# Performance work log

Measured on AMD Instinct MI355X. Metric: run time of the kernel, lower is better.

Reference implementation:

```python
import jax, jax.numpy as jnp
import numpy as np

EPS = 1e-6

def elu_fm(x):
    # elu(x) + 1
    return jax.nn.elu(x) + 1.0

def setup_inputs() -> dict:
    key = jax.random.key(0)
    k1, k2, k3 = jax.random.split(key, 3)
    N, L, H, D = 4, 4096, 16, 64
    queries = jax.random.normal(k1, (N, L, H, D), dtype=jnp.float32)
    keys = jax.random.normal(k2, (N, L, H, D), dtype=jnp.float32)
    values = jax.random.normal(k3, (N, L, H, D), dtype=jnp.float32)
    key_mask = jnp.ones((N, L), dtype=jnp.float32)
    return {"queries": queries, "keys": keys, "values": values, "key_mask": key_mask}

def reference(queries, keys, values, key_mask):
    Q = elu_fm(queries)                                  # [n, l, h, d]
    K = elu_fm(keys) * key_mask[:, :, None, None]        # [n, s, h, d]
    # KV accumulation: outer products of keys and values summed over sequence
    KV = jnp.einsum('nshd,nshm->nhmd', K, values)        # [n, h, m, d]
    # Normalizer: Q . sum_s K
    Z = 1.0 / (jnp.einsum('nlhd,nhd->nlh', Q, K.sum(axis=1)) + EPS)
    V = jnp.einsum('nlhd,nhmd,nlh->nlhm', Q, KV, Z)      # [n, l, h, m]
    return V
```

## Files before the change

kernel.cpp:

```cpp
#include <hip/hip_runtime.h>

#define EPS 1e-6f

typedef __attribute__((ext_vector_type(8))) short short8;
typedef __attribute__((ext_vector_type(16))) float f32x16;

__device__ __forceinline__ float elu1(float x) {
    return x > 0.f ? x + 1.f : __expf(x);
}

__device__ __forceinline__ short f2bf(float x) {
    unsigned u = __float_as_uint(x);
    return (short)((u + 0x7FFFu + ((u >> 16) & 1u)) >> 16);
}

#define LGKMCNT0() asm volatile("s_waitcnt lgkmcnt(0)" ::: "memory")
#define BAR() do { LGKMCNT0(); __builtin_amdgcn_s_barrier(); \
                   asm volatile("" ::: "memory"); } while (0)

template<int ITERS>
__global__ __launch_bounds__(256, 2) void kv_partial_kernel(
    const float* __restrict__ keys, const float* __restrict__ values,
    const float* __restrict__ mask, float* __restrict__ pkv,
    float* __restrict__ pks)
{
    __shared__ float Kls[64][64];
    __shared__ float Vls[64][64];
    __shared__ float Mls[ITERS * 64];

    const int nh = blockIdx.x, n = nh >> 4, h = nh & 15;
    const int chunk = blockIdx.y;
    const int t = threadIdx.x, wv = t >> 6, l = t & 63;
    const int half = l >> 5, col = l & 31;
    const int r0 = t >> 4, c4 = (t & 15) * 4;

    const int s0 = chunk * (ITERS * 64);
    const float* kb = keys   + ((size_t)(n * 4096 + s0) * 16 + h) * 64;
    const float* vb = values + ((size_t)(n * 4096 + s0) * 16 + h) * 64;

    if (t < ITERS * 16)
        *(float4*)&Mls[t * 4] = *(const float4*)(mask + n * 4096 + s0 + t * 4);

    f32x16 acc[2][2];
    #pragma unroll
    for (int a = 0; a < 2; ++a)
        #pragma unroll
        for (int b = 0; b < 2; ++b)
            #pragma unroll
            for (int r = 0; r < 16; ++r) acc[a][b][r] = 0.f;
    float4 ks4 = make_float4(0.f, 0.f, 0.f, 0.f);

    float4 kr[4], vr[4];
    #pragma unroll
    for (int k = 0; k < 4; ++k) {
        const size_t go = (size_t)(r0 + 16 * k) * 1024 + c4;
        kr[k] = *(const float4*)(kb + go);
        vr[k] = *(const float4*)(vb + go);
    }

    #pragma unroll
    for (int it = 0; it < ITERS; ++it) {
        BAR();
        #pragma unroll
        for (int k = 0; k < 4; ++k) {
            const float msk = Mls[it * 64 + r0 + 16 * k];
            float4 kk = kr[k];
            kk.x = elu1(kk.x) * msk; kk.y = elu1(kk.y) * msk;
            kk.z = elu1(kk.z) * msk; kk.w = elu1(kk.w) * msk;
            ks4.x += kk.x; ks4.y += kk.y; ks4.z += kk.z; ks4.w += kk.w;
            *(float4*)&Kls[r0 + 16 * k][c4] = kk;
            *(float4*)&Vls[r0 + 16 * k][c4] = vr[k];
        }
        BAR();
        if (it + 1 < ITERS) {
            #pragma unroll
            for (int k = 0; k < 4; ++k) {
                const size_t go = (size_t)(r0 + 16 * k + 64 * (it + 1)) * 1024 + c4;
                kr[k] = *(const float4*)(kb + go);
                vr[k] = *(const float4*)(vb + go);
            }
        }
        short8 ka0, ka1, va0, va1;
        #pragma unroll
        for (int j = 0; j < 8; ++j) {
            const int s = 16 * wv + 8 * half + j;
            ka0[j] = f2bf(Kls[s][col]);
            ka1[j] = f2bf(Kls[s][col + 32]);
            va0[j] = f2bf(Vls[s][col]);
            va1[j] = f2bf(Vls[s][col + 32]);
        }
        acc[0][0] = __builtin_amdgcn_mfma_f32_32x32x16_bf16(ka0, va0, acc[0][0], 0, 0, 0);
        acc[0][1] = __builtin_amdgcn_mfma_f32_32x32x16_bf16(ka0, va1, acc[0][1], 0, 0, 0);
        acc[1][0] = __builtin_amdgcn_mfma_f32_32x32x16_bf16(ka1, va0, acc[1][0], 0, 0, 0);
        acc[1][1] = __builtin_amdgcn_mfma_f32_32x32x16_bf16(ka1, va1, acc[1][1], 0, 0, 0);
    }

    BAR();
    *(float4*)&Kls[r0][c4] = ks4;
    BAR();
    if (t < 64) {
        float s = 0.f;
        #pragma unroll
        for (int r = 0; r < 16; ++r) s += Kls[r][t];
        pks[((size_t)chunk * 64 + nh) * 64 + t] = s;
    }
    BAR();

    float* cb0 = &Kls[0][0];
    float* cb1 = &Vls[0][0];
#define FLATW(BUF)                                                         \
    { _Pragma("unroll") for (int td = 0; td < 2; ++td)                     \
      _Pragma("unroll") for (int tm = 0; tm < 2; ++tm)                     \
      _Pragma("unroll") for (int r = 0; r < 16; ++r)                       \
          BUF[((td * 2 + tm) * 16 + r) * 64 + l] = acc[td][tm][r]; }
#define FLATR(BUF)                                                         \
    { _Pragma("unroll") for (int td = 0; td < 2; ++td)                     \
      _Pragma("unroll") for (int tm = 0; tm < 2; ++tm)                     \
      _Pragma("unroll") for (int r = 0; r < 16; ++r)                       \
          acc[td][tm][r] += BUF[((td * 2 + tm) * 16 + r) * 64 + l]; }
    if (wv == 2) FLATW(cb0);
    if (wv == 3) FLATW(cb1);
    BAR();
    if (wv == 0) FLATR(cb0);
    if (wv == 1) FLATR(cb1);
    BAR();
    if (wv == 1) FLATW(cb0);
    BAR();
    if (wv == 0) {
        FLATR(cb0);
        float* pb = pkv + ((size_t)chunk * 64 + nh) * 4096;
        #pragma unroll
        for (int td = 0; td < 2; ++td)
            #pragma unroll
            for (int tm = 0; tm < 2; ++tm)
                #pragma unroll
                for (int r = 0; r < 16; ++r) {
                    const int d = 32 * td + (r & 3) + 8 * (r >> 2) + 4 * half;
                    pb[(size_t)d * 64 + 32 * tm + col] = acc[td][tm][r];
                }
    }
#undef FLATW
#undef FLATR
}

__global__ __launch_bounds__(256) void kv_reduce_kernel(
    const float* __restrict__ pkv, const float* __restrict__ pks,
    float* __restrict__ kvt, float* __restrict__ ksum, int CH)
{
    const int nh = blockIdx.x;
    const int f4 = blockIdx.y * 256 + threadIdx.x;
    float4 s4 = make_float4(0.f, 0.f, 0.f, 0.f);
    #pragma unroll 4
    for (int c = 0; c < CH; ++c) {
        const float4 v = *(const float4*)(pkv + ((size_t)c * 64 + nh) * 4096 + f4 * 4);
        s4.x += v.x; s4.y += v.y; s4.z += v.z; s4.w += v.w;
    }
    *(float4*)(kvt + (size_t)nh * 4096 + f4 * 4) = s4;

    if (blockIdx.y == 0 && threadIdx.x < 64) {
        float s = 0.f;
        #pragma unroll 4
        for (int c = 0; c < CH; ++c)
            s += pks[((size_t)c * 64 + nh) * 64 + threadIdx.x];
        ksum[nh * 64 + threadIdx.x] = s;
    }
}

__global__ __launch_bounds__(256) void out_kernel(
    const float* __restrict__ queries, const float* __restrict__ kvt,
    const float* __restrict__ ksum, float* __restrict__ out)
{
    __shared__ float Qs[64][68];
    __shared__ float KVs[64][68];
    __shared__ float Ksm[64];

    const int nh = blockIdx.x;
    const int n = nh >> 4, h = nh & 15;
    const int t = threadIdx.x;
    const int l0 = blockIdx.y * 64;

    #pragma unroll
    for (int k = 0; k < 4; ++k) {
        const int idx = t + k * 256;
        *(float4*)&KVs[idx >> 4][(idx & 15) * 4] =
            *(const float4*)(kvt + (size_t)nh * 4096 + idx * 4);
    }
    if (t < 64) Ksm[t] = ksum[nh * 64 + t];

    #pragma unroll
    for (int k = 0; k < 4; ++k) {
        const int idx = t + k * 256;
        const int row = idx >> 4, seg = idx & 15;
        const size_t g = ((size_t)(n * 4096 + l0 + row) * 16 + h) * 64 + seg * 4;
        float4 q4 = *(const float4*)(queries + g);
        q4.x = elu1(q4.x);
        q4.y = elu1(q4.y);
        q4.z = elu1(q4.z);
        q4.w = elu1(q4.w);
        *(float4*)&Qs[row][seg * 4] = q4;
    }
    __syncthreads();

    const int mg = t & 7;
    const int lg = t >> 3;

    float acc[2][8];
    float zacc[2] = {0.f, 0.f};
    #pragma unroll
    for (int i = 0; i < 2; ++i)
        #pragma unroll
        for (int j = 0; j < 8; ++j) acc[i][j] = 0.f;

    #pragma unroll 4
    for (int d0 = 0; d0 < 64; d0 += 4) {
        const float4 km4 = *(const float4*)&Ksm[d0];
        float4 q[2];
        q[0] = *(const float4*)&Qs[lg][d0];
        q[1] = *(const float4*)&Qs[lg + 32][d0];
        #pragma unroll
        for (int i = 0; i < 2; ++i)
            zacc[i] += q[i].x * km4.x + q[i].y * km4.y +
                       q[i].z * km4.z + q[i].w * km4.w;
        #pragma unroll
        for (int r = 0; r < 4; ++r) {
            const float4 kva = *(const float4*)&KVs[d0 + r][mg * 4];
            const float4 kvb = *(const float4*)&KVs[d0 + r][32 + mg * 4];
            #pragma unroll
            for (int i = 0; i < 2; ++i) {
                const float qc = ((const float*)&q[i])[r];
                acc[i][0] = fmaf(qc, kva.x, acc[i][0]);
                acc[i][1] = fmaf(qc, kva.y, acc[i][1]);
                acc[i][2] = fmaf(qc, kva.z, acc[i][2]);
                acc[i][3] = fmaf(qc, kva.w, acc[i][3]);
                acc[i][4] = fmaf(qc, kvb.x, acc[i][4]);
                acc[i][5] = fmaf(qc, kvb.y, acc[i][5]);
                acc[i][6] = fmaf(qc, kvb.z, acc[i][6]);
                acc[i][7] = fmaf(qc, kvb.w, acc[i][7]);
            }
        }
    }

    #pragma unroll
    for (int i = 0; i < 2; ++i) {
        const float z = 1.f / (zacc[i] + EPS);
        const int row = l0 + lg + 32 * i;
        const size_t g = ((size_t)(n * 4096 + row) * 16 + h) * 64;
        float4 o;
        o.x = acc[i][0] * z; o.y = acc[i][1] * z;
        o.z = acc[i][2] * z; o.w = acc[i][3] * z;
        *(float4*)(out + g + mg * 4) = o;
        o.x = acc[i][4] * z; o.y = acc[i][5] * z;
        o.z = acc[i][6] * z; o.w = acc[i][7] * z;
        *(float4*)(out + g + 32 + mg * 4) = o;
    }
}

extern "C" void kernel_launch(void* const* d_in, const int* in_sizes, int n_in,
                              void* d_out, int out_size, void* d_ws, size_t ws_size,
                              hipStream_t stream) {
    const float* queries = (const float*)d_in[0];
    const float* keys    = (const float*)d_in[1];
    const float* values  = (const float*)d_in[2];
    const float* mask    = (const float*)d_in[3];
    float* out = (float*)d_out;

    auto need = [](int CH) {
        return ((size_t)CH * 64 * 4096 + (size_t)CH * 64 * 64 +
                (size_t)64 * 4096 + 64 * 64) * sizeof(float);
    };
    const int CH = (need(16) <= ws_size) ? 16 : 8;

    float* pkv  = (float*)d_ws;
    float* pks  = pkv + (size_t)CH * 64 * 4096;
    float* kvt  = pks + (size_t)CH * 64 * 64;
    float* ksum = kvt + (size_t)64 * 4096;

    if (CH == 16)
        kv_partial_kernel<4><<<dim3(64, 16), 256, 0, stream>>>(keys, values, mask, pkv, pks);
    else
        kv_partial_kernel<8><<<dim3(64, 8), 256, 0, stream>>>(keys, values, mask, pkv, pks);
    kv_reduce_kernel<<<dim3(64, 4), 256, 0, stream>>>(pkv, pks, kvt, ksum, CH);
    out_kernel<<<dim3(64, 64), 256, 0, stream>>>(queries, kvt, ksum, out);
}
```

Measured before the change: 79.76 us.

## Split KV accumulation into more sequence chunks and drop register prefetch pipeline

Raises the number of sequence chunks in the KV partial kernel from 16 to 64, so each block handles one 64-row tile, giving 4096 blocks instead of 1024. The register double-buffered prefetch and the shared-memory mask staging are removed; each iteration now loads its keys, values and mask straight from global memory, and the custom barrier macro is replaced with __syncthreads. The aim is more parallelism to hide memory latency on the bandwidth-bound partial pass. In exchange, the partial-KV workspace written to memory and read back by the reduce kernel grows fourfold, and each block pays a larger fixed epilogue cost for its cross-wave reduction.

New measurement: 103.6 us. +29.9%, slower.

```diff
diff --git a/kernel.cpp b/kernel.cpp
--- a/kernel.cpp
+++ b/kernel.cpp
@@ -13,10 +13,6 @@
     unsigned u = __float_as_uint(x);
     return (short)((u + 0x7FFFu + ((u >> 16) & 1u)) >> 16);
 }
-
-#define LGKMCNT0() asm volatile("s_waitcnt lgkmcnt(0)" ::: "memory")
-#define BAR() do { LGKMCNT0(); __builtin_amdgcn_s_barrier(); \
-                   asm volatile("" ::: "memory"); } while (0)
 
 template<int ITERS>
 __global__ __launch_bounds__(256, 2) void kv_partial_kernel(
@@ -26,7 +22,6 @@
 {
     __shared__ float Kls[64][64];
     __shared__ float Vls[64][64];
-    __shared__ float Mls[ITERS * 64];
 
     const int nh = blockIdx.x, n = nh >> 4, h = nh & 15;
     const int chunk = blockIdx.y;
@@ -37,9 +32,7 @@
     const int s0 = chunk * (ITERS * 64);
     const float* kb = keys   + ((size_t)(n * 4096 + s0) * 16 + h) * 64;
     const float* vb = values + ((size_t)(n * 4096 + s0) * 16 + h) * 64;
-
-    if (t < ITERS * 16)
-        *(float4*)&Mls[t * 4] = *(const float4*)(mask + n * 4096 + s0 + t * 4);
+    const float* mb = mask + n * 4096 + s0;
 
     f32x16 acc[2][2];
     #pragma unroll
@@ -50,36 +43,31 @@
             for (int r = 0; r < 16; ++r) acc[a][b][r] = 0.f;
     float4 ks4 = make_float4(0.f, 0.f, 0.f, 0.f);
 
-    float4 kr[4], vr[4];
-    #pragma unroll
-    for (int k = 0; k < 4; ++k) {
-        const size_t go = (size_t)(r0 + 16 * k) * 1024 + c4;
-        kr[k] = *(const float4*)(kb + go);
-        vr[k] = *(const float4*)(vb + go);
-    }
-
     #pragma unroll
     for (int it = 0; it < ITERS; ++it) {
-        BAR();
+        float4 kr[4], vr[4];
+        float mr[4];
         #pragma unroll
         for (int k = 0; k < 4; ++k) {
-            const float msk = Mls[it * 64 + r0 + 16 * k];
+            const int row = r0 + 16 * k;
+            const size_t go = (size_t)(it * 64 + row) * 1024 + c4;
+            kr[k] = *(const float4*)(kb + go);
+            vr[k] = *(const float4*)(vb + go);
+            mr[k] = mb[it * 64 + row];
+        }
+        if (it) __syncthreads();
+        #pragma unroll
+        for (int k = 0; k < 4; ++k) {
+            const int row = r0 + 16 * k;
             float4 kk = kr[k];
+            const float msk = mr[k];
             kk.x = elu1(kk.x) * msk; kk.y = elu1(kk.y) * msk;
             kk.z = elu1(kk.z) * msk; kk.w = elu1(kk.w) * msk;
             ks4.x += kk.x; ks4.y += kk.y; ks4.z += kk.z; ks4.w += kk.w;
-            *(float4*)&Kls[r0 + 16 * k][c4] = kk;
-            *(float4*)&Vls[r0 + 16 * k][c4] = vr[k];
-        }
-        BAR();
-        if (it + 1 < ITERS) {
-            #pragma unroll
-            for (int k = 0; k < 4; ++k) {
-                const size_t go = (size_t)(r0 + 16 * k + 64 * (it + 1)) * 1024 + c4;
-                kr[k] = *(const float4*)(kb + go);
-                vr[k] = *(const float4*)(vb + go);
-            }
-        }
+            *(float4*)&Kls[row][c4] = kk;
+            *(float4*)&Vls[row][c4] = vr[k];
+        }
+        __syncthreads();
         short8 ka0, ka1, va0, va1;
         #pragma unroll
         for (int j = 0; j < 8; ++j) {
@@ -95,16 +83,16 @@
         acc[1][1] = __builtin_amdgcn_mfma_f32_32x32x16_bf16(ka1, va1, acc[1][1], 0, 0, 0);
     }
 
-    BAR();
+    __syncthreads();
     *(float4*)&Kls[r0][c4] = ks4;
-    BAR();
+    __syncthreads();
     if (t < 64) {
         float s = 0.f;
         #pragma unroll
         for (int r = 0; r < 16; ++r) s += Kls[r][t];
         pks[((size_t)chunk * 64 + nh) * 64 + t] = s;
     }
-    BAR();
+    __syncthreads();
 
     float* cb0 = &Kls[0][0];
     float* cb1 = &Vls[0][0];
@@ -120,12 +108,12 @@
           acc[td][tm][r] += BUF[((td * 2 + tm) * 16 + r) * 64 + l]; }
     if (wv == 2) FLATW(cb0);
     if (wv == 3) FLATW(cb1);
-    BAR();
+    __syncthreads();
     if (wv == 0) FLATR(cb0);
     if (wv == 1) FLATR(cb1);
-    BAR();
+    __syncthreads();
     if (wv == 1) FLATW(cb0);
-    BAR();
+    __syncthreads();
     if (wv == 0) {
         FLATR(cb0);
         float* pb = pkv + ((size_t)chunk * 64 + nh) * 4096;
@@ -268,17 +256,17 @@
         return ((size_t)CH * 64 * 4096 + (size_t)CH * 64 * 64 +
                 (size_t)64 * 4096 + 64 * 64) * sizeof(float);
     };
-    const int CH = (need(16) <= ws_size) ? 16 : 8;
+    const int CH = (need(64) <= ws_size) ? 64 : 32;
 
     float* pkv  = (float*)d_ws;
     float* pks  = pkv + (size_t)CH * 64 * 4096;
     float* kvt  = pks + (size_t)CH * 64 * 64;
     float* ksum = kvt + (size_t)64 * 4096;
 
-    if (CH == 16)
-        kv_partial_kernel<4><<<dim3(64, 16), 256, 0, stream>>>(keys, values, mask, pkv, pks);
+    if (CH == 64)
+        kv_partial_kernel<1><<<dim3(64, 64), 256, 0, stream>>>(keys, values, mask, pkv, pks);
     else
-        kv_partial_kernel<8><<<dim3(64, 8), 256, 0, stream>>>(keys, values, mask, pkv, pks);
+        kv_partial_kernel<2><<<dim3(64, 32), 256, 0, stream>>>(keys, values, mask, pkv, pks);
     kv_reduce_kernel<<<dim3(64, 4), 256, 0, stream>>>(pkv, pks, kvt, ksum, CH);
     out_kernel<<<dim3(64, 64), 256, 0, stream>>>(queries, kvt, ksum, out);
 }
```

## Stage K/V as transposed bf16 in LDS and fix chunk count at 8

Applied to the files above, without the earlier changes.

K and V are now converted to bf16 once when written to shared memory, stored transposed with padding so each lane fetches its MFMA operand with two 8-byte LDS reads instead of 32 scalar float reads plus per-element conversion. Separate float buffers hold the cross-wave accumulator combine. The launcher now always uses 8 chunks of 8 iterations instead of 16 chunks when workspace allows, which halves partial-sum traffic but also halves grid parallelism in the first kernel. LDS footprint grows, which may affect occupancy at two blocks per CU.

New measurement: 73.76 us. 7.5% less time.

```diff
diff --git a/kernel.cpp b/kernel.cpp
--- a/kernel.cpp
+++ b/kernel.cpp
@@ -4,14 +4,19 @@
 
 typedef __attribute__((ext_vector_type(8))) short short8;
 typedef __attribute__((ext_vector_type(16))) float f32x16;
+typedef __attribute__((ext_vector_type(2))) unsigned int uint2v;
 
 __device__ __forceinline__ float elu1(float x) {
     return x > 0.f ? x + 1.f : __expf(x);
 }
 
-__device__ __forceinline__ short f2bf(float x) {
+__device__ __forceinline__ unsigned f2bfu(float x) {
     unsigned u = __float_as_uint(x);
-    return (short)((u + 0x7FFFu + ((u >> 16) & 1u)) >> 16);
+    return (u + 0x7FFFu + ((u >> 16) & 1u)) >> 16;
+}
+
+__device__ __forceinline__ float fidx(const float4& v, int i) {
+    return i == 0 ? v.x : i == 1 ? v.y : i == 2 ? v.z : v.w;
 }
 
 #define LGKMCNT0() asm volatile("s_waitcnt lgkmcnt(0)" ::: "memory")
@@ -24,8 +29,9 @@
     const float* __restrict__ mask, float* __restrict__ pkv,
     float* __restrict__ pks)
 {
-    __shared__ float Kls[64][64];
-    __shared__ float Vls[64][64];
+    __shared__ __align__(16) unsigned short KVbt[2][64][68];
+    __shared__ float cmbA[4096];
+    __shared__ float cmbB[4096];
     __shared__ float Mls[ITERS * 64];
 
     const int nh = blockIdx.x, n = nh >> 4, h = nh & 15;
@@ -41,6 +47,9 @@
     if (t < ITERS * 16)
         *(float4*)&Mls[t * 4] = *(const float4*)(mask + n * 4096 + s0 + t * 4);
 
+    char* kvbase = (char*)&KVbt[0][0][0];
+    const char* lbase = kvbase + col * 136 + 32 * wv + 16 * half;
+
     f32x16 acc[2][2];
     #pragma unroll
     for (int a = 0; a < 2; ++a)
@@ -61,6 +70,7 @@
     #pragma unroll
     for (int it = 0; it < ITERS; ++it) {
         BAR();
+        float4 kt[4];
         #pragma unroll
         for (int k = 0; k < 4; ++k) {
             const float msk = Mls[it * 64 + r0 + 16 * k];
@@ -68,8 +78,18 @@
             kk.x = elu1(kk.x) * msk; kk.y = elu1(kk.y) * msk;
             kk.z = elu1(kk.z) * msk; kk.w = elu1(kk.w) * msk;
             ks4.x += kk.x; ks4.y += kk.y; ks4.z += kk.z; ks4.w += kk.w;
-            *(float4*)&Kls[r0 + 16 * k][c4] = kk;
-            *(float4*)&Vls[r0 + 16 * k][c4] = vr[k];
+            kt[k] = kk;
+        }
+        #pragma unroll
+        for (int i = 0; i < 4; ++i) {
+            uint2v kw, vw;
+            kw[0] = f2bfu(fidx(kt[0], i)) | (f2bfu(fidx(kt[1], i)) << 16);
+            kw[1] = f2bfu(fidx(kt[2], i)) | (f2bfu(fidx(kt[3], i)) << 16);
+            vw[0] = f2bfu(fidx(vr[0], i)) | (f2bfu(fidx(vr[1], i)) << 16);
+            vw[1] = f2bfu(fidx(vr[2], i)) | (f2bfu(fidx(vr[3], i)) << 16);
+            const int bo = (c4 + i) * 136 + 8 * r0;
+            *(uint2v*)(kvbase + bo) = kw;
+            *(uint2v*)(kvbase + 8704 + bo) = vw;
         }
         BAR();
         if (it + 1 < ITERS) {
@@ -80,34 +100,35 @@
                 vr[k] = *(const float4*)(vb + go);
             }
         }
-        short8 ka0, ka1, va0, va1;
-        #pragma unroll
-        for (int j = 0; j < 8; ++j) {
-            const int s = 16 * wv + 8 * half + j;
-            ka0[j] = f2bf(Kls[s][col]);
-            ka1[j] = f2bf(Kls[s][col + 32]);
-            va0[j] = f2bf(Vls[s][col]);
-            va1[j] = f2bf(Vls[s][col + 32]);
-        }
-        acc[0][0] = __builtin_amdgcn_mfma_f32_32x32x16_bf16(ka0, va0, acc[0][0], 0, 0, 0);
-        acc[0][1] = __builtin_amdgcn_mfma_f32_32x32x16_bf16(ka0, va1, acc[0][1], 0, 0, 0);
-        acc[1][0] = __builtin_amdgcn_mfma_f32_32x32x16_bf16(ka1, va0, acc[1][0], 0, 0, 0);
-        acc[1][1] = __builtin_amdgcn_mfma_f32_32x32x16_bf16(ka1, va1, acc[1][1], 0, 0, 0);
-    }
-
-    BAR();
-    *(float4*)&Kls[r0][c4] = ks4;
+        union UF { uint2v u[2]; short8 s; };
+        UF ua, ub, uc, ud;
+        ua.u[0] = *(const uint2v*)(lbase + 0);
+        ua.u[1] = *(const uint2v*)(lbase + 8);
+        ub.u[0] = *(const uint2v*)(lbase + 4352);
+        ub.u[1] = *(const uint2v*)(lbase + 4360);
+        uc.u[0] = *(const uint2v*)(lbase + 8704);
+        uc.u[1] = *(const uint2v*)(lbase + 8712);
+        ud.u[0] = *(const uint2v*)(lbase + 13056);
+        ud.u[1] = *(const uint2v*)(lbase + 13064);
+        acc[0][0] = __builtin_amdgcn_mfma_f32_32x32x16_bf16(ua.s, uc.s, acc[0][0], 0, 0, 0);
+        acc[0][1] = __builtin_amdgcn_mfma_f32_32x32x16_bf16(ua.s, ud.s, acc[0][1], 0, 0, 0);
+        acc[1][0] = __builtin_amdgcn_mfma_f32_32x32x16_bf16(ub.s, uc.s, acc[1][0], 0, 0, 0);
+        acc[1][1] = __builtin_amdgcn_mfma_f32_32x32x16_bf16(ub.s, ud.s, acc[1][1], 0, 0, 0);
+    }
+
+    BAR();
+    *(float4*)&cmbA[r0 * 64 + c4] = ks4;
     BAR();
     if (t < 64) {
         float s = 0.f;
         #pragma unroll
-        for (int r = 0; r < 16; ++r) s += Kls[r][t];
+        for (int r = 0; r < 16; ++r) s += cmbA[r * 64 + t];
         pks[((size_t)chunk * 64 + nh) * 64 + t] = s;
     }
     BAR();
 
-    float* cb0 = &Kls[0][0];
-    float* cb1 = &Vls[0][0];
+    float* cb0 = cmbA;
+    float* cb1 = cmbB;
 #define FLATW(BUF)                                                         \
     { _Pragma("unroll") for (int td = 0; td < 2; ++td)                     \
       _Pragma("unroll") for (int tm = 0; tm < 2; ++tm)                     \
@@ -227,7 +248,7 @@
             const float4 kvb = *(const float4*)&KVs[d0 + r][32 + mg * 4];
             #pragma unroll
             for (int i = 0; i < 2; ++i) {
-                const float qc = ((const float*)&q[i])[r];
+                const float qc = fidx(q[i], r);
                 acc[i][0] = fmaf(qc, kva.x, acc[i][0]);
                 acc[i][1] = fmaf(qc, kva.y, acc[i][1]);
                 acc[i][2] = fmaf(qc, kva.z, acc[i][2]);
@@ -264,21 +285,15 @@
     const float* mask    = (const float*)d_in[3];
     float* out = (float*)d_out;
 
-    auto need = [](int CH) {
-        return ((size_t)CH * 64 * 4096 + (size_t)CH * 64 * 64 +
-                (size_t)64 * 4096 + 64 * 64) * sizeof(float);
-    };
-    const int CH = (need(16) <= ws_size) ? 16 : 8;
+    const int CH = 8;
 
     float* pkv  = (float*)d_ws;
     float* pks  = pkv + (size_t)CH * 64 * 4096;
     float* kvt  = pks + (size_t)CH * 64 * 64;
     float* ksum = kvt + (size_t)64 * 4096;
 
-    if (CH == 16)
-        kv_partial_kernel<4><<<dim3(64, 16), 256, 0, stream>>>(keys, values, mask, pkv, pks);
-    else
-        kv_partial_kernel<8><<<dim3(64, 8), 256, 0, stream>>>(keys, values, mask, pkv, pks);
+    kv_partial_kernel<8><<<dim3(64, CH), 256, 0, stream>>>(keys, values, mask,
+                                                           pkv, pks);
     kv_reduce_kernel<<<dim3(64, 4), 256, 0, stream>>>(pkv, pks, kvt, ksum, CH);
     out_kernel<<<dim3(64, 64), 256, 0, stream>>>(queries, kvt, ksum, out);
 }
```

## Replace bf16 MFMA KV accumulation with fp32 register-tiled FMA outer products

Applied to the files above, without the earlier changes.

The KV partial kernel drops the bf16 MFMA path and computes the K^T V outer-product sum in fp32 with per-thread 4x4 register tiles read from padded LDS. This removes the bf16 conversion and the cross-wave LDS reduction at the end, since each thread now writes its own tile directly. The reduce kernel scatters the results back into [d][m] order. It also drops the workspace-size fallback and always uses 16 chunks. The trade is more VALU FMA work in place of matrix-core throughput, plus uncoalesced scattered stores in the reduce kernel.

After: 100.0 us. 25.4% more time.

```diff
diff --git a/kernel.cpp b/kernel.cpp
--- a/kernel.cpp
+++ b/kernel.cpp
@@ -1,17 +1,13 @@
 #include <hip/hip_runtime.h>
 
 #define EPS 1e-6f
-
-typedef __attribute__((ext_vector_type(8))) short short8;
-typedef __attribute__((ext_vector_type(16))) float f32x16;
 
 __device__ __forceinline__ float elu1(float x) {
     return x > 0.f ? x + 1.f : __expf(x);
 }
 
-__device__ __forceinline__ short f2bf(float x) {
-    unsigned u = __float_as_uint(x);
-    return (short)((u + 0x7FFFu + ((u >> 16) & 1u)) >> 16);
+__device__ __forceinline__ float fidx(const float4& v, int i) {
+    return i == 0 ? v.x : i == 1 ? v.y : i == 2 ? v.z : v.w;
 }
 
 #define LGKMCNT0() asm volatile("s_waitcnt lgkmcnt(0)" ::: "memory")
@@ -24,15 +20,15 @@
     const float* __restrict__ mask, float* __restrict__ pkv,
     float* __restrict__ pks)
 {
-    __shared__ float Kls[64][64];
-    __shared__ float Vls[64][64];
+    __shared__ float Kls[64][68];
+    __shared__ float Vls[64][68];
     __shared__ float Mls[ITERS * 64];
 
     const int nh = blockIdx.x, n = nh >> 4, h = nh & 15;
     const int chunk = blockIdx.y;
-    const int t = threadIdx.x, wv = t >> 6, l = t & 63;
-    const int half = l >> 5, col = l & 31;
+    const int t = threadIdx.x;
     const int r0 = t >> 4, c4 = (t & 15) * 4;
+    const int m0 = (t >> 4) * 4, d0 = (t & 15) * 4;
 
     const int s0 = chunk * (ITERS * 64);
     const float* kb = keys   + ((size_t)(n * 4096 + s0) * 16 + h) * 64;
@@ -41,13 +37,11 @@
     if (t < ITERS * 16)
         *(float4*)&Mls[t * 4] = *(const float4*)(mask + n * 4096 + s0 + t * 4);
 
-    f32x16 acc[2][2];
-    #pragma unroll
-    for (int a = 0; a < 2; ++a)
-        #pragma unroll
-        for (int b = 0; b < 2; ++b)
-            #pragma unroll
-            for (int r = 0; r < 16; ++r) acc[a][b][r] = 0.f;
+    float acc[4][4];
+    #pragma unroll
+    for (int i = 0; i < 4; ++i)
+        #pragma unroll
+        for (int j = 0; j < 4; ++j) acc[i][j] = 0.f;
     float4 ks4 = make_float4(0.f, 0.f, 0.f, 0.f);
 
     float4 kr[4], vr[4];
@@ -80,19 +74,19 @@
                 vr[k] = *(const float4*)(vb + go);
             }
         }
-        short8 ka0, ka1, va0, va1;
-        #pragma unroll
-        for (int j = 0; j < 8; ++j) {
-            const int s = 16 * wv + 8 * half + j;
-            ka0[j] = f2bf(Kls[s][col]);
-            ka1[j] = f2bf(Kls[s][col + 32]);
-            va0[j] = f2bf(Vls[s][col]);
-            va1[j] = f2bf(Vls[s][col + 32]);
-        }
-        acc[0][0] = __builtin_amdgcn_mfma_f32_32x32x16_bf16(ka0, va0, acc[0][0], 0, 0, 0);
-        acc[0][1] = __builtin_amdgcn_mfma_f32_32x32x16_bf16(ka0, va1, acc[0][1], 0, 0, 0);
-        acc[1][0] = __builtin_amdgcn_mfma_f32_32x32x16_bf16(ka1, va0, acc[1][0], 0, 0, 0);
-        acc[1][1] = __builtin_amdgcn_mfma_f32_32x32x16_bf16(ka1, va1, acc[1][1], 0, 0, 0);
+        #pragma unroll 4
+        for (int s = 0; s < 64; ++s) {
+            const float4 vv = *(const float4*)&Vls[s][m0];
+            const float4 kk = *(const float4*)&Kls[s][d0];
+            #pragma unroll
+            for (int i = 0; i < 4; ++i) {
+                const float vi = fidx(vv, i);
+                acc[i][0] = fmaf(vi, kk.x, acc[i][0]);
+                acc[i][1] = fmaf(vi, kk.y, acc[i][1]);
+                acc[i][2] = fmaf(vi, kk.z, acc[i][2]);
+                acc[i][3] = fmaf(vi, kk.w, acc[i][3]);
+            }
+        }
     }
 
     BAR();
@@ -104,43 +98,13 @@
         for (int r = 0; r < 16; ++r) s += Kls[r][t];
         pks[((size_t)chunk * 64 + nh) * 64 + t] = s;
     }
-    BAR();
-
-    float* cb0 = &Kls[0][0];
-    float* cb1 = &Vls[0][0];
-#define FLATW(BUF)                                                         \
-    { _Pragma("unroll") for (int td = 0; td < 2; ++td)                     \
-      _Pragma("unroll") for (int tm = 0; tm < 2; ++tm)                     \
-      _Pragma("unroll") for (int r = 0; r < 16; ++r)                       \
-          BUF[((td * 2 + tm) * 16 + r) * 64 + l] = acc[td][tm][r]; }
-#define FLATR(BUF)                                                         \
-    { _Pragma("unroll") for (int td = 0; td < 2; ++td)                     \
-      _Pragma("unroll") for (int tm = 0; tm < 2; ++tm)                     \
-      _Pragma("unroll") for (int r = 0; r < 16; ++r)                       \
-          acc[td][tm][r] += BUF[((td * 2 + tm) * 16 + r) * 64 + l]; }
-    if (wv == 2) FLATW(cb0);
-    if (wv == 3) FLATW(cb1);
-    BAR();
-    if (wv == 0) FLATR(cb0);
-    if (wv == 1) FLATR(cb1);
-    BAR();
-    if (wv == 1) FLATW(cb0);
-    BAR();
-    if (wv == 0) {
-        FLATR(cb0);
-        float* pb = pkv + ((size_t)chunk * 64 + nh) * 4096;
-        #pragma unroll
-        for (int td = 0; td < 2; ++td)
-            #pragma unroll
-            for (int tm = 0; tm < 2; ++tm)
-                #pragma unroll
-                for (int r = 0; r < 16; ++r) {
-                    const int d = 32 * td + (r & 3) + 8 * (r >> 2) + 4 * half;
-                    pb[(size_t)d * 64 + 32 * tm + col] = acc[td][tm][r];
-                }
-    }
-#undef FLATW
-#undef FLATR
+
+    float* pb = pkv + ((size_t)chunk * 64 + nh) * 4096;
+    #pragma unroll
+    for (int i = 0; i < 4; ++i)
+        #pragma unroll
+        for (int j = 0; j < 4; ++j)
+            pb[(i * 4 + j) * 256 + t] = acc[i][j];
 }
 
 __global__ __launch_bounds__(256) void kv_reduce_kernel(
@@ -155,7 +119,16 @@
         const float4 v = *(const float4*)(pkv + ((size_t)c * 64 + nh) * 4096 + f4 * 4);
         s4.x += v.x; s4.y += v.y; s4.z += v.z; s4.w += v.w;
     }
-    *(float4*)(kvt + (size_t)nh * 4096 + f4 * 4) = s4;
+    const float vals[4] = {s4.x, s4.y, s4.z, s4.w};
+    const int k = f4 >> 6;
+    const int tb = (f4 & 63) * 4;
+    #pragma unroll
+    for (int u = 0; u < 4; ++u) {
+        const int t = tb + u;
+        const int m = ((t >> 4) << 2) + (k >> 2);
+        const int d = ((t & 15) << 2) + (k & 3);
+        kvt[(size_t)nh * 4096 + d * 64 + m] = vals[u];
+    }
 
     if (blockIdx.y == 0 && threadIdx.x < 64) {
         float s = 0.f;
@@ -227,7 +200,7 @@
             const float4 kvb = *(const float4*)&KVs[d0 + r][32 + mg * 4];
             #pragma unroll
             for (int i = 0; i < 2; ++i) {
-                const float qc = ((const float*)&q[i])[r];
+                const float qc = fidx(q[i], r);
                 acc[i][0] = fmaf(qc, kva.x, acc[i][0]);
                 acc[i][1] = fmaf(qc, kva.y, acc[i][1]);
                 acc[i][2] = fmaf(qc, kva.z, acc[i][2]);
@@ -264,21 +237,15 @@
     const float* mask    = (const float*)d_in[3];
     float* out = (float*)d_out;
 
-    auto need = [](int CH) {
-        return ((size_t)CH * 64 * 4096 + (size_t)CH * 64 * 64 +
-                (size_t)64 * 4096 + 64 * 64) * sizeof(float);
-    };
-    const int CH = (need(16) <= ws_size) ? 16 : 8;
+    const int CH = 16;
 
     float* pkv  = (float*)d_ws;
     float* pks  = pkv + (size_t)CH * 64 * 4096;
     float* kvt  = pks + (size_t)CH * 64 * 64;
     float* ksum = kvt + (size_t)64 * 4096;
 
-    if (CH == 16)
-        kv_partial_kernel<4><<<dim3(64, 16), 256, 0, stream>>>(keys, values, mask, pkv, pks);
-    else
-        kv_partial_kernel<8><<<dim3(64, 8), 256, 0, stream>>>(keys, values, mask, pkv, pks);
+    kv_partial_kernel<4><<<dim3(64, CH), 256, 0, stream>>>(keys, values, mask,
+                                                           pkv, pks);
     kv_reduce_kernel<<<dim3(64, 4), 256, 0, stream>>>(pkv, pks, kvt, ksum, CH);
     out_kernel<<<dim3(64, 64), 256, 0, stream>>>(queries, kvt, ksum, out);
 }
```
